# Optimization experiments

Hardware: AMD Instinct MI355X
Metric: run time of the kernel (lower is better)

Reference implementation:

```python
import jax, jax.numpy as jnp
import numpy as np

D_MODEL, NHEAD, D_HIDDEN, N_EXPERTS, TOP_K = 1024, 16, 4096, 8, 2
HEAD_DIM = D_MODEL // NHEAD
LN_EPS = 1e-5


def _layernorm(x, g, b):
    mu = jnp.mean(x, axis=-1, keepdims=True)
    var = jnp.mean((x - mu) ** 2, axis=-1, keepdims=True)
    return (x - mu) * jax.lax.rsqrt(var + LN_EPS) * g + b


def setup_inputs() -> dict:
    key = jax.random.key(0)
    ks = jax.random.split(key, 12)
    s = 0.02
    return {
        "src": jax.random.normal(ks[0], (4, 2048, D_MODEL), dtype=jnp.float32),
        "in_proj_w": jax.random.normal(ks[1], (3 * D_MODEL, D_MODEL), dtype=jnp.float32) * s,
        "in_proj_b": jnp.zeros((3 * D_MODEL,), jnp.float32),
        "out_proj_w": jax.random.normal(ks[2], (D_MODEL, D_MODEL), dtype=jnp.float32) * s,
        "out_proj_b": jnp.zeros((D_MODEL,), jnp.float32),
        "ln1_g": jnp.ones((D_MODEL,), jnp.float32),
        "ln1_b": jnp.zeros((D_MODEL,), jnp.float32),
        "gate_w": jax.random.normal(ks[3], (N_EXPERTS, D_MODEL), dtype=jnp.float32) * s,
        "gate_b": jnp.zeros((N_EXPERTS,), jnp.float32),
        "w1": jax.random.normal(ks[4], (N_EXPERTS, D_HIDDEN, D_MODEL), dtype=jnp.float32) * s,
        "b1": jnp.zeros((N_EXPERTS, D_HIDDEN), jnp.float32),
        "w2": jax.random.normal(ks[5], (N_EXPERTS, D_MODEL, D_HIDDEN), dtype=jnp.float32) * s,
        "b2": jnp.zeros((N_EXPERTS, D_MODEL), jnp.float32),
        "ln2_g": jnp.ones((D_MODEL,), jnp.float32),
        "ln2_b": jnp.zeros((D_MODEL,), jnp.float32),
    }


def _forward(src, in_proj_w, in_proj_b, out_proj_w, out_proj_b,
             ln1_g, ln1_b, gate_w, gate_b, w1, b1, w2, b2, ln2_g, ln2_b):
    B, S, D = src.shape
    # --- multihead self-attention (torch nn.MultiheadAttention semantics) ---
    qkv = src @ in_proj_w.T + in_proj_b                       # [B,S,3D]
    q, k, v = jnp.split(qkv, 3, axis=-1)
    def heads(t):
        return t.reshape(B, S, NHEAD, HEAD_DIM).transpose(0, 2, 1, 3)  # [B,H,S,hd]
    q, k, v = heads(q), heads(k), heads(v)
    scores = jnp.einsum("bhqd,bhkd->bhqk", q, k) / jnp.sqrt(jnp.float32(HEAD_DIM))
    attn = jax.nn.softmax(scores, axis=-1)
    ctx = jnp.einsum("bhqk,bhkd->bhqd", attn, v)
    ctx = ctx.transpose(0, 2, 1, 3).reshape(B, S, D)
    attn_out = ctx @ out_proj_w.T + out_proj_b
    x = _layernorm(src + attn_out, ln1_g, ln1_b)
    # --- MoE FFN: linear gate, top-k softmax routing, 2-layer ReLU experts ---
    xt = x.reshape(B * S, D)                                  # [T,D]
    gating_logits = xt @ gate_w.T + gate_b                    # [T,E]
    top_vals, top_idx = jax.lax.top_k(gating_logits, TOP_K)   # [T,k]
    top_probs = jax.nn.softmax(top_vals, axis=-1)             # [T,k]
    # dense [T,E] routing weights (zero for non-selected experts)
    weights = jnp.sum(top_probs[..., None] * jax.nn.one_hot(top_idx, N_EXPERTS, dtype=xt.dtype), axis=1)
    moe = jnp.zeros_like(xt)
    for e in range(N_EXPERTS):  # small fixed loop over experts
        h = jax.nn.relu(xt @ w1[e].T + b1[e])                 # [T,d_hidden]
        moe = moe + weights[:, e:e + 1] * (h @ w2[e].T + b2[e])
    moe = moe.reshape(B, S, D)
    out = _layernorm(x + moe, ln2_g, ln2_b)
    return out, gating_logits.reshape(B, S, N_EXPERTS)


def reference(src, in_proj_w, in_proj_b, out_proj_w, out_proj_b,
              ln1_g, ln1_b, gate_w, gate_b, w1, b1, w2, b2, ln2_g, ln2_b):
    return _forward(src, in_proj_w, in_proj_b, out_proj_w, out_proj_b,
                    ln1_g, ln1_b, gate_w, gate_b, w1, b1, w2, b2, ln2_g, ln2_b)
```

## Files before the change

kernel.cpp:

```cpp
#include <hip/hip_runtime.h>
#include <cstdint>

#define DEV static __device__ __forceinline__

typedef unsigned short u16;
typedef unsigned int   u32;
typedef __attribute__((ext_vector_type(8))) short bf16x8;
typedef __attribute__((ext_vector_type(8))) _Float16 f16x8;
typedef __attribute__((ext_vector_type(4))) float f32x4;

constexpr int TT   = 8192;
constexpr int DM   = 1024;
constexpr int DHID = 4096;
constexpr int MPAD = 17408;

constexpr size_t OFF_R0 = 0;
constexpr size_t OFF_R1 = 142606336;
constexpr size_t OFF_R2 = 178257920;
constexpr size_t OFF_R3 = 211812352;
constexpr size_t OFF_RT = 247463936;

DEV u16 f2b(float f){ u32 b = __builtin_bit_cast(u32, f); return (u16)((b + 0x7FFFu + ((b>>16)&1u))>>16); }
DEV float b2f(u16 u){ u32 b = ((u32)u)<<16; return __builtin_bit_cast(float, b); }

DEV void split2(float x, float y, u32& hi, u32& lo){
  _Float16 hx = (_Float16)x, hy = (_Float16)y;
  float rx = (x - (float)hx)*1024.f, ry = (y - (float)hy)*1024.f;
  _Float16 lx = (_Float16)rx, ly = (_Float16)ry;
  hi = (u32)__builtin_bit_cast(u16,hx) | ((u32)__builtin_bit_cast(u16,hy)<<16);
  lo = (u32)__builtin_bit_cast(u16,lx) | ((u32)__builtin_bit_cast(u16,ly)<<16);
}

DEV void stage16(const float* __restrict__ src, u16* hiB, u16* loB, int r, int c0, float scale){
  float4 v[4];
  #pragma unroll
  for (int j=0;j<4;j++) v[j] = *(const float4*)(src + c0 + 4*j);
  #pragma unroll
  for (int j=0;j<4;j++){ v[j].x*=scale; v[j].y*=scale; v[j].z*=scale; v[j].w*=scale; }
  u32 h[8], lo8[8];
  split2(v[0].x, v[0].y, h[0], lo8[0]); split2(v[0].z, v[0].w, h[1], lo8[1]);
  split2(v[1].x, v[1].y, h[2], lo8[2]); split2(v[1].z, v[1].w, h[3], lo8[3]);
  split2(v[2].x, v[2].y, h[4], lo8[4]); split2(v[2].z, v[2].w, h[5], lo8[5]);
  split2(v[3].x, v[3].y, h[6], lo8[6]); split2(v[3].z, v[3].w, h[7], lo8[7]);
  const int cb = c0>>3;
  const int i0 = r*64 + (((cb+0) ^ (r&7))<<3);
  const int i1 = r*64 + (((cb+1) ^ (r&7))<<3);
  *(uint4*)&hiB[i0] = make_uint4(h[0],h[1],h[2],h[3]);
  *(uint4*)&hiB[i1] = make_uint4(h[4],h[5],h[6],h[7]);
  *(uint4*)&loB[i0] = make_uint4(lo8[0],lo8[1],lo8[2],lo8[3]);
  *(uint4*)&loB[i1] = make_uint4(lo8[4],lo8[5],lo8[6],lo8[7]);
}

template<int RESID>
__global__ __launch_bounds__(256,2) void gemm_f16x2_kernel(
    const float* __restrict__ A, const float* __restrict__ W,
    const float* __restrict__ bias, const float* __restrict__ resid,
    float* __restrict__ C, int K, int N)
{
  __shared__ __align__(16) u16 sm[24576];
  u16* Ahi = sm;          u16* Alo = sm + 8192;
  u16* Bhi = sm + 16384;  u16* Blo = sm + 20480;
  const int m0 = blockIdx.y*128, n0 = blockIdx.x*64;
  const int t = threadIdx.x, l = t&63, w = t>>6;
  const int lr = l&15, lg = l>>4;
  const int wr = (w>>1)*64, wc = (w&1)*32;
  const int ar = t>>1, ac0 = (t&1)*32;
  const int br = t>>2, bc0 = (t&3)*16;
  f32x4 a0[4][2], a1[4][2];
  #pragma unroll
  for (int m=0;m<4;m++)
    #pragma unroll
    for (int n=0;n<2;n++){ a0[m][n]=(f32x4){0,0,0,0}; a1[m][n]=(f32x4){0,0,0,0}; }
  const float* Arow = A + (size_t)(m0+ar)*K;
  const float* Wrow = W + (size_t)(n0+br)*K;
  for (int k0=0; k0<K; k0+=64){
    __syncthreads();
    stage16(Arow + k0, Ahi, Alo, ar, ac0,      1.f);
    stage16(Arow + k0, Ahi, Alo, ar, ac0 + 16, 1.f);
    stage16(Wrow + k0, Bhi, Blo, br, bc0,      1.f);
    __syncthreads();
    #pragma unroll
    for (int s=0;s<2;s++){
      f16x8 bh[2], bl[2];
      #pragma unroll
      for (int n=0;n<2;n++){
        const int bi = (wc+16*n+lr)*64 + ((32*s + 8*lg) ^ ((lr&7)<<3));
        bh[n] = *(const f16x8*)&Bhi[bi];
        bl[n] = *(const f16x8*)&Blo[bi];
      }
      #pragma unroll
      for (int m=0;m<4;m++){
        const int ai = (wr+16*m+lr)*64 + ((32*s + 8*lg) ^ ((lr&7)<<3));
        const f16x8 ah = *(const f16x8*)&Ahi[ai];
        const f16x8 al = *(const f16x8*)&Alo[ai];
        #pragma unroll
        for (int n=0;n<2;n++){
          a0[m][n] = __builtin_amdgcn_mfma_f32_16x16x32_f16(ah, bh[n], a0[m][n], 0,0,0);
          a1[m][n] = __builtin_amdgcn_mfma_f32_16x16x32_f16(ah, bl[n], a1[m][n], 0,0,0);
          a1[m][n] = __builtin_amdgcn_mfma_f32_16x16x32_f16(al, bh[n], a1[m][n], 0,0,0);
        }
      }
    }
  }
  #pragma unroll
  for (int m=0;m<4;m++)
    #pragma unroll
    for (int n=0;n<2;n++){
      const int gn = n0 + wc + 16*n + lr;
      const float be = bias[gn];
      #pragma unroll
      for (int r=0;r<4;r++){
        const int gm = m0 + wr + 16*m + 4*lg + r;
        float v = a0[m][n][r] + a1[m][n][r]*9.765625e-4f + be;
        if (RESID) v += resid[(size_t)gm*N + gn];
        C[(size_t)gm*N + gn] = v;
      }
    }
}

__global__ __launch_bounds__(256,2) void attn_mfma_kernel(
    const float* __restrict__ qkv, float* __restrict__ ctx)
{
  __shared__ __align__(16) u16 sm[24576];
  u16* Khi = sm;          u16* Klo = sm + 4096;
  u16* Vhi = sm + 8192;   u16* Vlo = sm + 12288;
  u16* Phi = sm + 16384;  u16* Plo = sm + 20480;
  float* fsm = (float*)sm;
  const int bh = blockIdx.y, bb = bh>>4, h = bh&15;
  const int tb = bb*2048, q0 = blockIdx.x*64, go = h*64;
  const int t = threadIdx.x, l = t&63, w = t>>6;
  const int lr = l&15, lg = l>>4;
  const int sr = t>>2, sc0 = (t&3)*16;

  stage16(qkv + (size_t)(tb+q0+sr)*3072 + go, Phi, Plo, sr, sc0, 0.125f);
  __syncthreads();
  f16x8 qh[2], ql[2];
  #pragma unroll
  for (int s=0;s<2;s++){
    const int qi = (16*w+lr)*64 + ((32*s + 8*lg) ^ ((lr&7)<<3));
    qh[s] = *(const f16x8*)&Phi[qi];
    ql[s] = *(const f16x8*)&Plo[qi];
  }

  float m_ = -1e30f, l_ = 0.f;
  f32x4 c0a[4], c1a[4];
  #pragma unroll
  for (int m=0;m<4;m++){ c0a[m]=(f32x4){0,0,0,0}; c1a[m]=(f32x4){0,0,0,0}; }

  for (int kt=0; kt<32; ++kt){
    const size_t kb = (size_t)(tb + kt*64);
    __syncthreads();
    stage16(qkv + (kb+sr)*3072 + 1024 + go, Khi, Klo, sr, sc0, 1.f);
    {
      const int d = l;
      u32 vh[8], vlo[8];
      #pragma unroll
      for (int j=0;j<8;j++){
        const float f0 = qkv[(kb + w*16 + 2*j    )*3072 + 2048 + go + d];
        const float f1 = qkv[(kb + w*16 + 2*j + 1)*3072 + 2048 + go + d];
        split2(f0, f1, vh[j], vlo[j]);
      }
      const int i0 = d*64 + ((16*w + 0) ^ ((d&7)<<3));
      const int i1 = d*64 + ((16*w + 8) ^ ((d&7)<<3));
      *(uint4*)&Vhi[i0] = make_uint4(vh[0],vh[1],vh[2],vh[3]);
      *(uint4*)&Vhi[i1] = make_uint4(vh[4],vh[5],vh[6],vh[7]);
      *(uint4*)&Vlo[i0] = make_uint4(vlo[0],vlo[1],vlo[2],vlo[3]);
      *(uint4*)&Vlo[i1] = make_uint4(vlo[4],vlo[5],vlo[6],vlo[7]);
    }
    __syncthreads();
    f32x4 s0[4], s1[4];
    #pragma unroll
    for (int m=0;m<4;m++){ s0[m]=(f32x4){0,0,0,0}; s1[m]=(f32x4){0,0,0,0}; }
    #pragma unroll
    for (int s=0;s<2;s++){
      #pragma unroll
      for (int m=0;m<4;m++){
        const int ai = (16*m+lr)*64 + ((32*s + 8*lg) ^ ((lr&7)<<3));
        const f16x8 ah = *(const f16x8*)&Khi[ai];
        const f16x8 al = *(const f16x8*)&Klo[ai];
        s0[m] = __builtin_amdgcn_mfma_f32_16x16x32_f16(ah, qh[s], s0[m], 0,0,0);
        s1[m] = __builtin_amdgcn_mfma_f32_16x16x32_f16(ah, ql[s], s1[m], 0,0,0);
        s1[m] = __builtin_amdgcn_mfma_f32_16x16x32_f16(al, qh[s], s1[m], 0,0,0);
      }
    }
    float p[4][4];
    float mx = -1e30f;
    #pragma unroll
    for (int m=0;m<4;m++)
      #pragma unroll
      for (int r=0;r<4;r++){
        const float v = s0[m][r] + s1[m][r]*9.765625e-4f;
        p[m][r] = v; mx = fmaxf(mx, v);
      }
    mx = fmaxf(mx, __shfl_xor(mx,16));
    mx = fmaxf(mx, __shfl_xor(mx,32));
    const float mn = fmaxf(m_, mx);
    const float sc = __expf(m_ - mn);
    float rs = 0.f;
    #pragma unroll
    for (int m=0;m<4;m++)
      #pragma unroll
      for (int r=0;r<4;r++){ const float e = __expf(p[m][r]-mn); p[m][r]=e; rs += e; }
    rs += __shfl_xor(rs,16);
    rs += __shfl_xor(rs,32);
    l_ = l_*sc + rs; m_ = mn;
    #pragma unroll
    for (int m=0;m<4;m++){ c0a[m] *= sc; c1a[m] *= sc; }
    const int prow = 16*w + lr;
    #pragma unroll
    for (int m=0;m<4;m++){
      u32 h0,l0,h1,l1;
      split2(p[m][0], p[m][1], h0, l0);
      split2(p[m][2], p[m][3], h1, l1);
      const int pi = prow*64 + ((16*m + 4*lg) ^ ((lr&7)<<3));
      *(uint2*)&Phi[pi] = make_uint2(h0,h1);
      *(uint2*)&Plo[pi] = make_uint2(l0,l1);
    }
    #pragma unroll
    for (int s=0;s<2;s++){
      const int bi = prow*64 + ((32*s + 8*lg) ^ ((lr&7)<<3));
      const f16x8 ph = *(const f16x8*)&Phi[bi];
      const f16x8 pl = *(const f16x8*)&Plo[bi];
      #pragma unroll
      for (int m=0;m<4;m++){
        const int ai = (16*m+lr)*64 + ((32*s + 8*lg) ^ ((lr&7)<<3));
        const f16x8 vh8 = *(const f16x8*)&Vhi[ai];
        const f16x8 vl8 = *(const f16x8*)&Vlo[ai];
        c0a[m] = __builtin_amdgcn_mfma_f32_16x16x32_f16(vh8, ph, c0a[m], 0,0,0);
        c1a[m] = __builtin_amdgcn_mfma_f32_16x16x32_f16(vh8, pl, c1a[m], 0,0,0);
        c1a[m] = __builtin_amdgcn_mfma_f32_16x16x32_f16(vl8, ph, c1a[m], 0,0,0);
      }
    }
  }
  __syncthreads();
  {
    const float inv = 1.f/l_;
    const int q = 16*w + lr;
    #pragma unroll
    for (int m=0;m<4;m++)
      #pragma unroll
      for (int r=0;r<4;r++)
        fsm[q*68 + 16*m + 4*lg + r] = (c0a[m][r] + c1a[m][r]*9.765625e-4f)*inv;
  }
  __syncthreads();
  #pragma unroll
  for (int j=0;j<4;j++){
    const float4 vv = *(const float4*)&fsm[sr*68 + sc0 + 4*j];
    *(float4*)&ctx[(size_t)(tb+q0+sr)*1024 + go + sc0 + 4*j] = vv;
  }
}

__global__ __launch_bounds__(256) void ln_kernel(const float* __restrict__ in,
    const float* __restrict__ g, const float* __restrict__ b, float* __restrict__ o)
{
  const int r = blockIdx.x, t = threadIdx.x;
  const float4 v = *(const float4*)&in[(size_t)r*1024 + t*4];
  float s = v.x+v.y+v.z+v.w;
  float q = v.x*v.x + v.y*v.y + v.z*v.z + v.w*v.w;
  #pragma unroll
  for (int off=1; off<64; off<<=1){ s += __shfl_xor(s,off); q += __shfl_xor(q,off); }
  __shared__ float red[8];
  const int w = t>>6, lane = t&63;
  if (lane==0){ red[w]=s; red[4+w]=q; }
  __syncthreads();
  s = red[0]+red[1]+red[2]+red[3];
  q = red[4]+red[5]+red[6]+red[7];
  const float mu = s*(1.f/1024.f);
  const float var = q*(1.f/1024.f) - mu*mu;
  const float rstd = rsqrtf(var + 1e-5f);
  const float4 gv = *(const float4*)&g[t*4];
  const float4 bv = *(const float4*)&b[t*4];
  *(float4*)&o[(size_t)r*1024 + t*4] = make_float4(
    (v.x-mu)*rstd*gv.x + bv.x, (v.y-mu)*rstd*gv.y + bv.y,
    (v.z-mu)*rstd*gv.z + bv.z, (v.w-mu)*rstd*gv.w + bv.w);
}

__global__ __launch_bounds__(256) void gate_kernel(
    const float* __restrict__ xf, const float* __restrict__ gw, const float* __restrict__ gb,
    float* __restrict__ glog, int* __restrict__ top2e,
    float* __restrict__ p0a, float* __restrict__ p1a, int* __restrict__ counts)
{
  const int tok  = blockIdx.x*4 + (threadIdx.x>>6);
  const int lane = threadIdx.x & 63;
  float part[8] = {};
  const float* xr = xf + (size_t)tok*1024;
  #pragma unroll
  for (int kk=0; kk<16; kk++){
    const int d = kk*64 + lane;
    const float xv = xr[d];
    #pragma unroll
    for (int e=0;e<8;e++) part[e] = fmaf(xv, gw[e*1024+d], part[e]);
  }
  #pragma unroll
  for (int e=0;e<8;e++){
    float s = part[e];
    s += __shfl_xor(s,1); s += __shfl_xor(s,2); s += __shfl_xor(s,4);
    s += __shfl_xor(s,8); s += __shfl_xor(s,16); s += __shfl_xor(s,32);
    part[e] = s + gb[e];
  }
  if (lane==0){
    #pragma unroll
    for (int e=0;e<8;e++) glog[(size_t)tok*8+e] = part[e];
    float v0=-1e30f; int e0=0;
    #pragma unroll
    for (int e=0;e<8;e++) if (part[e] > v0){ v0=part[e]; e0=e; }
    float v1=-1e30f; int e1=0;
    #pragma unroll
    for (int e=0;e<8;e++) if (e!=e0 && part[e] > v1){ v1=part[e]; e1=e; }
    const float p0 = 1.f/(1.f + __expf(v1-v0));
    top2e[tok] = e0 | (e1<<4);
    p0a[tok] = p0; p1a[tok] = 1.f - p0;
    atomicAdd(&counts[e0],1); atomicAdd(&counts[e1],1);
  }
}

__global__ void route_offsets_kernel(const int* __restrict__ counts, int* __restrict__ offs,
                                     int* __restrict__ cursors, int* __restrict__ rowmap)
{
  const int t = threadIdx.x;
  if (t==0){
    int a=0;
    for (int e=0;e<8;e++){ offs[e]=a; a += (counts[e]+127)&~127; }
    offs[8]=a;
  }
  if (t<8) cursors[t]=0;
  for (int i=t;i<MPAD;i+=256) rowmap[i] = -1;
}

__global__ void route_assign_kernel(const int* __restrict__ top2e, const int* __restrict__ offs,
    int* __restrict__ cursors, int* __restrict__ rowmap, int* __restrict__ tokslot)
{
  const int tok = blockIdx.x*256 + threadIdx.x;
  const int pk = top2e[tok];
  const int e0 = pk & 15, e1 = pk >> 4;
  const int s0 = offs[e0] + atomicAdd(&cursors[e0], 1);
  const int s1 = offs[e1] + atomicAdd(&cursors[e1], 1);
  rowmap[s0] = tok; rowmap[s1] = tok;
  tokslot[2*tok] = s0; tokslot[2*tok+1] = s1;
}

__global__ __launch_bounds__(256) void gather_kernel(const int* __restrict__ rowmap,
    const float* __restrict__ xf, u16* __restrict__ xg)
{
  const int slot = blockIdx.x, t = threadIdx.x;
  u16* dst = xg + (size_t)slot*1024;
  const int r = rowmap[slot];
  if (r >= 0){
    const float4 v = *(const float4*)&xf[(size_t)r*1024 + t*4];
    uint2 p; p.x = (u32)f2b(v.x) | ((u32)f2b(v.y)<<16);
             p.y = (u32)f2b(v.z) | ((u32)f2b(v.w)<<16);
    *(uint2*)&dst[t*4] = p;
  } else {
    uint2 z; z.x=0u; z.y=0u;
    *(uint2*)&dst[t*4] = z;
  }
}

template<int KDIM, int EPI>
__global__ __launch_bounds__(256,2) void gemm_moe_kernel(
    const u16* __restrict__ A, const float* __restrict__ Wbase,
    const float* __restrict__ biasbase, u16* __restrict__ C,
    const int* __restrict__ offs, int N)
{
  constexpr int LS = 56;
  __shared__ u16 As[128*LS];
  __shared__ u16 Bs[128*LS];
  const int m0 = blockIdx.y*128, n0 = blockIdx.x*128;
  int e = 0;
  #pragma unroll
  for (int i=1;i<8;i++) if (offs[i] <= m0) e = i;
  const float* W    = Wbase + (size_t)e*N*KDIM;
  const float* bias = biasbase + (size_t)e*N;
  const int t = threadIdx.x;
  const int w = t>>6, lane = t&63;
  const int wr = (w>>1)*64, wc = (w&1)*64;
  const int lr = lane&15, lk = (lane>>4)*8;
  const int ar = t>>2, ac8 = (t&3)*8;
  const int br = t>>3, bc4 = (t&7)*4;
  f32x4 acc[4][4];
  #pragma unroll
  for (int mi=0;mi<4;mi++)
    #pragma unroll
    for (int ni=0;ni<4;ni++){ acc[mi][ni][0]=0.f; acc[mi][ni][1]=0.f; acc[mi][ni][2]=0.f; acc[mi][ni][3]=0.f; }
  for (int k0=0; k0<KDIM; k0+=32){
    __syncthreads();
    #pragma unroll
    for (int it=0; it<2; it++){
      const int r = ar + it*64;
      *(uint4*)&As[r*LS + ac8] = *(const uint4*)&A[(size_t)(m0+r)*KDIM + k0 + ac8];
    }
    #pragma unroll
    for (int it=0; it<4; it++){
      const int r = br + it*32;
      const float4 v = *(const float4*)&W[(size_t)(n0+r)*KDIM + k0 + bc4];
      uint2 p; p.x = (u32)f2b(v.x) | ((u32)f2b(v.y)<<16);
               p.y = (u32)f2b(v.z) | ((u32)f2b(v.w)<<16);
      *(uint2*)&Bs[r*LS + bc4] = p;
    }
    __syncthreads();
    bf16x8 af[4], bfr[4];
    #pragma unroll
    for (int mi=0;mi<4;mi++) af[mi]  = *(const bf16x8*)&As[(wr+mi*16+lr)*LS + lk];
    #pragma unroll
    for (int ni=0;ni<4;ni++) bfr[ni] = *(const bf16x8*)&Bs[(wc+ni*16+lr)*LS + lk];
    #pragma unroll
    for (int mi=0;mi<4;mi++)
      #pragma unroll
      for (int ni=0;ni<4;ni++)
        acc[mi][ni] = __builtin_amdgcn_mfma_f32_16x16x32_bf16(af[mi], bfr[ni], acc[mi][ni], 0,0,0);
  }
  const int lr4 = (lane>>4)*4, lc = lane&15;
  #pragma unroll
  for (int mi=0;mi<4;mi++)
    #pragma unroll
    for (int ni=0;ni<4;ni++){
      const int gn = n0 + wc + ni*16 + lc;
      const float be = bias[gn];
      #pragma unroll
      for (int j=0;j<4;j++){
        const int gm = m0 + wr + mi*16 + lr4 + j;
        float v = acc[mi][ni][j] + be;
        if (EPI==0) v = fmaxf(v, 0.f);
        C[(size_t)gm*N + gn] = f2b(v);
      }
    }
}

__global__ __launch_bounds__(256) void combine_ln2_kernel(
    const float* __restrict__ xf, const u16* __restrict__ y, const int* __restrict__ tokslot,
    const float* __restrict__ p0a, const float* __restrict__ p1a,
    const float* __restrict__ g, const float* __restrict__ b, float* __restrict__ o)
{
  const int tok = blockIdx.x, t = threadIdx.x;
  const int s0 = tokslot[2*tok], s1 = tokslot[2*tok+1];
  const float w0 = p0a[tok], w1 = p1a[tok];
  const float4 xv = *(const float4*)&xf[(size_t)tok*1024 + t*4];
  const uint2 ya = *(const uint2*)&y[(size_t)s0*1024 + t*4];
  const uint2 yb = *(const uint2*)&y[(size_t)s1*1024 + t*4];
  const float va[4] = {b2f((u16)(ya.x&0xFFFF)), b2f((u16)(ya.x>>16)),
                       b2f((u16)(ya.y&0xFFFF)), b2f((u16)(ya.y>>16))};
  const float vb[4] = {b2f((u16)(yb.x&0xFFFF)), b2f((u16)(yb.x>>16)),
                       b2f((u16)(yb.y&0xFFFF)), b2f((u16)(yb.y>>16))};
  const float xe[4] = {xv.x, xv.y, xv.z, xv.w};
  float vv[4];
  #pragma unroll
  for (int i=0;i<4;i++) vv[i] = xe[i] + w0*va[i] + w1*vb[i];
  float s = vv[0]+vv[1]+vv[2]+vv[3];
  float q = vv[0]*vv[0]+vv[1]*vv[1]+vv[2]*vv[2]+vv[3]*vv[3];
  #pragma unroll
  for (int off=1; off<64; off<<=1){ s += __shfl_xor(s,off); q += __shfl_xor(q,off); }
  __shared__ float red[8];
  const int w = t>>6, lane = t&63;
  if (lane==0){ red[w]=s; red[4+w]=q; }
  __syncthreads();
  s = red[0]+red[1]+red[2]+red[3];
  q = red[4]+red[5]+red[6]+red[7];
  const float mu = s*(1.f/1024.f);
  const float var = q*(1.f/1024.f) - mu*mu;
  const float rstd = rsqrtf(var + 1e-5f);
  const float4 gv = *(const float4*)&g[t*4];
  const float4 bv = *(const float4*)&b[t*4];
  *(float4*)&o[(size_t)tok*1024 + t*4] = make_float4(
    (vv[0]-mu)*rstd*gv.x + bv.x, (vv[1]-mu)*rstd*gv.y + bv.y,
    (vv[2]-mu)*rstd*gv.z + bv.z, (vv[3]-mu)*rstd*gv.w + bv.w);
}

extern "C" void kernel_launch(void* const* d_in, const int* in_sizes, int n_in,
                              void* d_out, int out_size, void* d_ws, size_t ws_size,
                              hipStream_t stream)
{
  const float* src  = (const float*)d_in[0];
  const float* inw  = (const float*)d_in[1];
  const float* inb  = (const float*)d_in[2];
  const float* ow   = (const float*)d_in[3];
  const float* ob   = (const float*)d_in[4];
  const float* ln1g = (const float*)d_in[5];
  const float* ln1b = (const float*)d_in[6];
  const float* gw   = (const float*)d_in[7];
  const float* gb   = (const float*)d_in[8];
  const float* w1   = (const float*)d_in[9];
  const float* b1   = (const float*)d_in[10];
  const float* w2   = (const float*)d_in[11];
  const float* b2   = (const float*)d_in[12];
  const float* ln2g = (const float*)d_in[13];
  const float* ln2b = (const float*)d_in[14];

  float* out  = (float*)d_out;
  float* glog = out + (size_t)TT*DM;

  char* ws = (char*)d_ws;
  float* qkvf    = (float*)(ws + OFF_R0);
  float* attnout = (float*)(ws + OFF_R0);
  u16*   hbuf    = (u16*)  (ws + OFF_R0);
  float* ctxf    = (float*)(ws + OFF_R1);
  u16*   ybuf    = (u16*)  (ws + OFF_R1);
  float* xf      = (float*)(ws + OFF_R2);
  u16*   xg      = (u16*)  (ws + OFF_R3);
  int*   top2e   = (int*)  (ws + OFF_RT);
  float* p0a     = (float*)(ws + OFF_RT + 32768);
  float* p1a     = (float*)(ws + OFF_RT + 65536);
  int*   counts  = (int*)  (ws + OFF_RT + 98304);
  int*   offs    = (int*)  (ws + OFF_RT + 98336);
  int*   cursors = (int*)  (ws + OFF_RT + 98400);
  int*   rowmap  = (int*)  (ws + OFF_RT + 98432);
  int*   tokslot = (int*)  (ws + OFF_RT + 168064);

  hipMemsetAsync(counts, 0, 8*sizeof(int), stream);

  gemm_f16x2_kernel<0><<<dim3(48,64),256,0,stream>>>(src, inw, inb, nullptr, qkvf, 1024, 3072);
  attn_mfma_kernel<<<dim3(32,64),256,0,stream>>>(qkvf, ctxf);
  gemm_f16x2_kernel<1><<<dim3(16,64),256,0,stream>>>(ctxf, ow, ob, src, attnout, 1024, 1024);
  ln_kernel<<<8192,256,0,stream>>>(attnout, ln1g, ln1b, xf);
  gate_kernel<<<2048,256,0,stream>>>(xf, gw, gb, glog, top2e, p0a, p1a, counts);
  route_offsets_kernel<<<1,256,0,stream>>>(counts, offs, cursors, rowmap);
  route_assign_kernel<<<32,256,0,stream>>>(top2e, offs, cursors, rowmap, tokslot);
  gather_kernel<<<MPAD,256,0,stream>>>(rowmap, xf, xg);
  gemm_moe_kernel<1024,0><<<dim3(32,136),256,0,stream>>>(xg, w1, b1, hbuf, offs, DHID);
  gemm_moe_kernel<4096,1><<<dim3(8,136),256,0,stream>>>(hbuf, w2, b2, ybuf, offs, DM);
  combine_ln2_kernel<<<8192,256,0,stream>>>(xf, ybuf, tokslot, p0a, p1a, ln2g, ln2b, out);
}
```

Baseline: 1.821 ms.

## Pre-split fp16 hi/lo operands once and stage via global_load_lds in attention GEMMs

Adds prep kernels that split src, in_proj and out_proj weights into pre-swizzled fp16 hi/lo arrays, and has the QKV GEMM epilogue emit split, swizzled Q/K plus an fp32 V that a transpose kernel turns into split V^T. The GEMMs and attention kernel then stage tiles straight from global to LDS with global_load_lds, with no per-tile conversion in the inner loop. The attention kernel writes its context already split for the out-projection. The cost is extra launches and extra workspace traffic for the split copies, including re-splitting the constant weights on every call.

Result: faster. 1.671 ms (-8.3%).

```diff
diff --git a/kernel.cpp b/kernel.cpp
--- a/kernel.cpp
+++ b/kernel.cpp
@@ -14,11 +14,27 @@
 constexpr int DHID = 4096;
 constexpr int MPAD = 17408;
 
-constexpr size_t OFF_R0 = 0;
-constexpr size_t OFF_R1 = 142606336;
-constexpr size_t OFF_R2 = 178257920;
-constexpr size_t OFF_R3 = 211812352;
-constexpr size_t OFF_RT = 247463936;
+constexpr size_t O_HBUF = 0;
+constexpr size_t O_XG   = 142606336;
+constexpr size_t O_YBUF = 178257920;
+constexpr size_t O_XF   = 213909504;
+constexpr size_t O_RT   = 247463936;
+constexpr size_t O_SRCH = 0;
+constexpr size_t O_SRCL = 16777216;
+constexpr size_t O_INWH = 33554432;
+constexpr size_t O_INWL = 39845888;
+constexpr size_t O_OWH  = 46137344;
+constexpr size_t O_OWL  = 48234496;
+constexpr size_t O_QH   = 50331648;
+constexpr size_t O_QL   = 67108864;
+constexpr size_t O_KH   = 83886080;
+constexpr size_t O_KL   = 100663296;
+constexpr size_t O_VF   = 117440512;
+constexpr size_t O_VTH  = 150994944;
+constexpr size_t O_VTL  = 167772160;
+constexpr size_t O_CTXH = 184549376;
+constexpr size_t O_CTXL = 201326592;
+constexpr size_t O_AOUT = 0;
 
 DEV u16 f2b(float f){ u32 b = __builtin_bit_cast(u32, f); return (u16)((b + 0x7FFFu + ((b>>16)&1u))>>16); }
 DEV float b2f(u16 u){ u32 b = ((u32)u)<<16; return __builtin_bit_cast(float, b); }
@@ -30,69 +46,127 @@
   hi = (u32)__builtin_bit_cast(u16,hx) | ((u32)__builtin_bit_cast(u16,hy)<<16);
   lo = (u32)__builtin_bit_cast(u16,lx) | ((u32)__builtin_bit_cast(u16,ly)<<16);
 }
-
-DEV void stage16(const float* __restrict__ src, u16* hiB, u16* loB, int r, int c0, float scale){
-  float4 v[4];
-  #pragma unroll
-  for (int j=0;j<4;j++) v[j] = *(const float4*)(src + c0 + 4*j);
-  #pragma unroll
-  for (int j=0;j<4;j++){ v[j].x*=scale; v[j].y*=scale; v[j].z*=scale; v[j].w*=scale; }
-  u32 h[8], lo8[8];
-  split2(v[0].x, v[0].y, h[0], lo8[0]); split2(v[0].z, v[0].w, h[1], lo8[1]);
-  split2(v[1].x, v[1].y, h[2], lo8[2]); split2(v[1].z, v[1].w, h[3], lo8[3]);
-  split2(v[2].x, v[2].y, h[4], lo8[4]); split2(v[2].z, v[2].w, h[5], lo8[5]);
-  split2(v[3].x, v[3].y, h[6], lo8[6]); split2(v[3].z, v[3].w, h[7], lo8[7]);
-  const int cb = c0>>3;
-  const int i0 = r*64 + (((cb+0) ^ (r&7))<<3);
-  const int i1 = r*64 + (((cb+1) ^ (r&7))<<3);
-  *(uint4*)&hiB[i0] = make_uint4(h[0],h[1],h[2],h[3]);
-  *(uint4*)&hiB[i1] = make_uint4(h[4],h[5],h[6],h[7]);
-  *(uint4*)&loB[i0] = make_uint4(lo8[0],lo8[1],lo8[2],lo8[3]);
-  *(uint4*)&loB[i1] = make_uint4(lo8[4],lo8[5],lo8[6],lo8[7]);
-}
-
-template<int RESID>
-__global__ __launch_bounds__(256,2) void gemm_f16x2_kernel(
-    const float* __restrict__ A, const float* __restrict__ W,
+DEV void split1(float x, u16& h, u16& l){
+  _Float16 hx = (_Float16)x;
+  float rx = (x - (float)hx)*1024.f;
+  h = __builtin_bit_cast(u16, hx);
+  l = __builtin_bit_cast(u16, (_Float16)rx);
+}
+
+DEV void gld16(const u16* g, u16* l){
+  __builtin_amdgcn_global_load_lds(
+    (const __attribute__((address_space(1))) void*)g,
+    (__attribute__((address_space(3))) void*)l, 16, 0, 0);
+}
+
+__global__ __launch_bounds__(256) void prep_split_kernel(
+    const float* __restrict__ src, u16* __restrict__ hi, u16* __restrict__ lo)
+{
+  const int g = blockIdx.x*256 + threadIdx.x;
+  const int r = g >> 7;
+  const int ci = g & 127;
+  const float4 v0 = *(const float4*)&src[(size_t)r*1024 + ci*8];
+  const float4 v1 = *(const float4*)&src[(size_t)r*1024 + ci*8 + 4];
+  u32 h[4], l4[4];
+  split2(v0.x,v0.y,h[0],l4[0]); split2(v0.z,v0.w,h[1],l4[1]);
+  split2(v1.x,v1.y,h[2],l4[2]); split2(v1.z,v1.w,h[3],l4[3]);
+  const int co = (ci & ~7) | ((ci ^ r) & 7);
+  *(uint4*)&hi[(size_t)r*1024 + co*8] = make_uint4(h[0],h[1],h[2],h[3]);
+  *(uint4*)&lo[(size_t)r*1024 + co*8] = make_uint4(l4[0],l4[1],l4[2],l4[3]);
+}
+
+__global__ __launch_bounds__(256) void prep_vt_kernel(
+    const float* __restrict__ Vf, u16* __restrict__ VTh, u16* __restrict__ VTl)
+{
+  __shared__ float fsm[64*65];
+  const int bh = blockIdx.x, st = blockIdx.y;
+  const int bb = bh>>4, h = bh&15, go = h*64;
+  const int s0 = bb*2048 + st*64;
+  const int t = threadIdx.x;
+  {
+    const int r = t>>2, c0 = (t&3)*16;
+    #pragma unroll
+    for (int j=0;j<4;j++){
+      const float4 v = *(const float4*)&Vf[(size_t)(s0+r)*1024 + go + c0 + 4*j];
+      fsm[r*65 + c0 + 4*j+0]=v.x; fsm[r*65 + c0 + 4*j+1]=v.y;
+      fsm[r*65 + c0 + 4*j+2]=v.z; fsm[r*65 + c0 + 4*j+3]=v.w;
+    }
+  }
+  __syncthreads();
+  const int d = t>>2, qs = t&3;
+  #pragma unroll
+  for (int j2=0;j2<2;j2++){
+    const int q = qs*2 + j2;
+    float v[8];
+    #pragma unroll
+    for (int jj=0;jj<8;jj++) v[jj] = fsm[(q*8+jj)*65 + d];
+    u32 h0,h1,h2,h3,l0,l1,l2,l3;
+    split2(v[0],v[1],h0,l0); split2(v[2],v[3],h1,l1);
+    split2(v[4],v[5],h2,l2); split2(v[6],v[7],h3,l3);
+    const int cst = q ^ (d&7);
+    const size_t base = (size_t)(bh*64 + d)*2048 + st*64 + cst*8;
+    *(uint4*)&VTh[base] = make_uint4(h0,h1,h2,h3);
+    *(uint4*)&VTl[base] = make_uint4(l0,l1,l2,l3);
+  }
+}
+
+template<int EPI>
+__global__ __launch_bounds__(256,2) void gemm_pair_kernel(
+    const u16* __restrict__ Ahi, const u16* __restrict__ Alo,
+    const u16* __restrict__ Bhi, const u16* __restrict__ Blo,
     const float* __restrict__ bias, const float* __restrict__ resid,
-    float* __restrict__ C, int K, int N)
+    float* __restrict__ outf,
+    u16* __restrict__ Qh, u16* __restrict__ Ql,
+    u16* __restrict__ Kh, u16* __restrict__ Kl, float* __restrict__ Vf,
+    int K, int N)
 {
   __shared__ __align__(16) u16 sm[24576];
-  u16* Ahi = sm;          u16* Alo = sm + 8192;
-  u16* Bhi = sm + 16384;  u16* Blo = sm + 20480;
+  u16* As_hi = sm;
+  u16* As_lo = sm + 8192;
+  u16* Bs_hi = sm + 16384;
+  u16* Bs_lo = sm + 20480;
   const int m0 = blockIdx.y*128, n0 = blockIdx.x*64;
   const int t = threadIdx.x, l = t&63, w = t>>6;
   const int lr = l&15, lg = l>>4;
   const int wr = (w>>1)*64, wc = (w&1)*32;
-  const int ar = t>>1, ac0 = (t&1)*32;
-  const int br = t>>2, bc0 = (t&3)*16;
+  const int srow = w*8 + (l>>3);
+  const int sch  = l&7;
   f32x4 a0[4][2], a1[4][2];
   #pragma unroll
   for (int m=0;m<4;m++)
     #pragma unroll
     for (int n=0;n<2;n++){ a0[m][n]=(f32x4){0,0,0,0}; a1[m][n]=(f32x4){0,0,0,0}; }
-  const float* Arow = A + (size_t)(m0+ar)*K;
-  const float* Wrow = W + (size_t)(n0+br)*K;
   for (int k0=0; k0<K; k0+=64){
     __syncthreads();
-    stage16(Arow + k0, Ahi, Alo, ar, ac0,      1.f);
-    stage16(Arow + k0, Ahi, Alo, ar, ac0 + 16, 1.f);
-    stage16(Wrow + k0, Bhi, Blo, br, bc0,      1.f);
+    #pragma unroll
+    for (int op=0; op<4; ++op){
+      const int r = op*32 + srow;
+      const size_t src = (size_t)(m0+r)*K + k0 + sch*8;
+      gld16(&Ahi[src], &As_hi[(op*32 + w*8)*64]);
+      gld16(&Alo[src], &As_lo[(op*32 + w*8)*64]);
+    }
+    #pragma unroll
+    for (int op=0; op<2; ++op){
+      const int r = op*32 + srow;
+      const size_t src = (size_t)(n0+r)*K + k0 + sch*8;
+      gld16(&Bhi[src], &Bs_hi[(op*32 + w*8)*64]);
+      gld16(&Blo[src], &Bs_lo[(op*32 + w*8)*64]);
+    }
     __syncthreads();
     #pragma unroll
     for (int s=0;s<2;s++){
       f16x8 bh[2], bl[2];
       #pragma unroll
       for (int n=0;n<2;n++){
-        const int bi = (wc+16*n+lr)*64 + ((32*s + 8*lg) ^ ((lr&7)<<3));
-        bh[n] = *(const f16x8*)&Bhi[bi];
-        bl[n] = *(const f16x8*)&Blo[bi];
+        const int bi = (wc+16*n+lr)*64 + (((4*s+lg) ^ (lr&7))<<3);
+        bh[n] = *(const f16x8*)&Bs_hi[bi];
+        bl[n] = *(const f16x8*)&Bs_lo[bi];
       }
       #pragma unroll
       for (int m=0;m<4;m++){
-        const int ai = (wr+16*m+lr)*64 + ((32*s + 8*lg) ^ ((lr&7)<<3));
-        const f16x8 ah = *(const f16x8*)&Ahi[ai];
-        const f16x8 al = *(const f16x8*)&Alo[ai];
+        const int ai = (wr+16*m+lr)*64 + (((4*s+lg) ^ (lr&7))<<3);
+        const f16x8 ah = *(const f16x8*)&As_hi[ai];
+        const f16x8 al = *(const f16x8*)&As_lo[ai];
         #pragma unroll
         for (int n=0;n<2;n++){
           a0[m][n] = __builtin_amdgcn_mfma_f32_16x16x32_f16(ah, bh[n], a0[m][n], 0,0,0);
@@ -103,43 +177,64 @@
     }
   }
   #pragma unroll
-  for (int m=0;m<4;m++)
-    #pragma unroll
-    for (int n=0;n<2;n++){
-      const int gn = n0 + wc + 16*n + lr;
-      const float be = bias[gn];
+  for (int n2=0;n2<2;n2++){
+    const int gn = n0 + wc + 16*n2 + lr;
+    const float be = bias[gn];
+    #pragma unroll
+    for (int m=0;m<4;m++){
       #pragma unroll
       for (int r=0;r<4;r++){
         const int gm = m0 + wr + 16*m + 4*lg + r;
-        float v = a0[m][n][r] + a1[m][n][r]*9.765625e-4f + be;
-        if (RESID) v += resid[(size_t)gm*N + gn];
-        C[(size_t)gm*N + gn] = v;
+        float v = a0[m][n2][r] + a1[m][n2][r]*9.765625e-4f + be;
+        if (EPI==0){
+          if (gn < 1024){
+            u16 hh,ll; split1(v*0.125f, hh, ll);
+            Qh[(size_t)gm*1024 + gn] = hh; Ql[(size_t)gm*1024 + gn] = ll;
+          } else if (gn < 2048){
+            const int c = gn - 1024;
+            const int cst = (c & ~63) | ((((c>>3) ^ gm) & 7)<<3) | (c & 7);
+            u16 hh,ll; split1(v, hh, ll);
+            Kh[(size_t)gm*1024 + cst] = hh; Kl[(size_t)gm*1024 + cst] = ll;
+          } else {
+            Vf[(size_t)gm*1024 + (gn-2048)] = v;
+          }
+        } else {
+          outf[(size_t)gm*N + gn] = v + resid[(size_t)gm*N + gn];
+        }
       }
     }
+  }
 }
 
 __global__ __launch_bounds__(256,2) void attn_mfma_kernel(
-    const float* __restrict__ qkv, float* __restrict__ ctx)
+    const u16* __restrict__ Qhp, const u16* __restrict__ Qlp,
+    const u16* __restrict__ Khp, const u16* __restrict__ Klp,
+    const u16* __restrict__ VTh, const u16* __restrict__ VTl,
+    u16* __restrict__ ctxh, u16* __restrict__ ctxl)
 {
   __shared__ __align__(16) u16 sm[24576];
-  u16* Khi = sm;          u16* Klo = sm + 4096;
-  u16* Vhi = sm + 8192;   u16* Vlo = sm + 12288;
-  u16* Phi = sm + 16384;  u16* Plo = sm + 20480;
+  u16* Khs = sm;
+  u16* Kls = sm + 4096;
+  u16* Vhs = sm + 8192;
+  u16* Vls = sm + 12288;
+  u16* Phs = sm + 16384;
+  u16* Pls = sm + 20480;
   float* fsm = (float*)sm;
   const int bh = blockIdx.y, bb = bh>>4, h = bh&15;
   const int tb = bb*2048, q0 = blockIdx.x*64, go = h*64;
   const int t = threadIdx.x, l = t&63, w = t>>6;
   const int lr = l&15, lg = l>>4;
-  const int sr = t>>2, sc0 = (t&3)*16;
-
-  stage16(qkv + (size_t)(tb+q0+sr)*3072 + go, Phi, Plo, sr, sc0, 0.125f);
-  __syncthreads();
+  const int srow = w*8 + (l>>3);
+  const int sch  = l&7;
+
   f16x8 qh[2], ql[2];
-  #pragma unroll
-  for (int s=0;s<2;s++){
-    const int qi = (16*w+lr)*64 + ((32*s + 8*lg) ^ ((lr&7)<<3));
-    qh[s] = *(const f16x8*)&Phi[qi];
-    ql[s] = *(const f16x8*)&Plo[qi];
+  {
+    const size_t qr = (size_t)(tb + q0 + 16*w + lr)*1024 + go;
+    #pragma unroll
+    for (int s=0;s<2;s++){
+      qh[s] = *(const f16x8*)&Qhp[qr + 32*s + 8*lg];
+      ql[s] = *(const f16x8*)&Qlp[qr + 32*s + 8*lg];
+    }
   }
 
   float m_ = -1e30f, l_ = 0.f;
@@ -148,24 +243,17 @@
   for (int m=0;m<4;m++){ c0a[m]=(f32x4){0,0,0,0}; c1a[m]=(f32x4){0,0,0,0}; }
 
   for (int kt=0; kt<32; ++kt){
-    const size_t kb = (size_t)(tb + kt*64);
+    const int kb = tb + kt*64;
     __syncthreads();
-    stage16(qkv + (kb+sr)*3072 + 1024 + go, Khi, Klo, sr, sc0, 1.f);
-    {
-      const int d = l;
-      u32 vh[8], vlo[8];
-      #pragma unroll
-      for (int j=0;j<8;j++){
-        const float f0 = qkv[(kb + w*16 + 2*j    )*3072 + 2048 + go + d];
-        const float f1 = qkv[(kb + w*16 + 2*j + 1)*3072 + 2048 + go + d];
-        split2(f0, f1, vh[j], vlo[j]);
-      }
-      const int i0 = d*64 + ((16*w + 0) ^ ((d&7)<<3));
-      const int i1 = d*64 + ((16*w + 8) ^ ((d&7)<<3));
-      *(uint4*)&Vhi[i0] = make_uint4(vh[0],vh[1],vh[2],vh[3]);
-      *(uint4*)&Vhi[i1] = make_uint4(vh[4],vh[5],vh[6],vh[7]);
-      *(uint4*)&Vlo[i0] = make_uint4(vlo[0],vlo[1],vlo[2],vlo[3]);
-      *(uint4*)&Vlo[i1] = make_uint4(vlo[4],vlo[5],vlo[6],vlo[7]);
+    #pragma unroll
+    for (int op=0; op<2; ++op){
+      const int r = op*32 + srow;
+      const size_t ksrc = (size_t)(kb + r)*1024 + go + sch*8;
+      const size_t vsrc = (size_t)(bh*64 + r)*2048 + kt*64 + sch*8;
+      gld16(&Khp[ksrc], &Khs[(op*32 + w*8)*64]);
+      gld16(&Klp[ksrc], &Kls[(op*32 + w*8)*64]);
+      gld16(&VTh[vsrc], &Vhs[(op*32 + w*8)*64]);
+      gld16(&VTl[vsrc], &Vls[(op*32 + w*8)*64]);
     }
     __syncthreads();
     f32x4 s0[4], s1[4];
@@ -175,9 +263,9 @@
     for (int s=0;s<2;s++){
       #pragma unroll
       for (int m=0;m<4;m++){
-        const int ai = (16*m+lr)*64 + ((32*s + 8*lg) ^ ((lr&7)<<3));
-        const f16x8 ah = *(const f16x8*)&Khi[ai];
-        const f16x8 al = *(const f16x8*)&Klo[ai];
+        const int ai = (16*m+lr)*64 + (((4*s+lg) ^ (lr&7))<<3);
+        const f16x8 ah = *(const f16x8*)&Khs[ai];
+        const f16x8 al = *(const f16x8*)&Kls[ai];
         s0[m] = __builtin_amdgcn_mfma_f32_16x16x32_f16(ah, qh[s], s0[m], 0,0,0);
         s1[m] = __builtin_amdgcn_mfma_f32_16x16x32_f16(ah, ql[s], s1[m], 0,0,0);
         s1[m] = __builtin_amdgcn_mfma_f32_16x16x32_f16(al, qh[s], s1[m], 0,0,0);
@@ -213,19 +301,19 @@
       split2(p[m][0], p[m][1], h0, l0);
       split2(p[m][2], p[m][3], h1, l1);
       const int pi = prow*64 + ((16*m + 4*lg) ^ ((lr&7)<<3));
-      *(uint2*)&Phi[pi] = make_uint2(h0,h1);
-      *(uint2*)&Plo[pi] = make_uint2(l0,l1);
+      *(uint2*)&Phs[pi] = make_uint2(h0,h1);
+      *(uint2*)&Pls[pi] = make_uint2(l0,l1);
     }
     #pragma unroll
     for (int s=0;s<2;s++){
       const int bi = prow*64 + ((32*s + 8*lg) ^ ((lr&7)<<3));
-      const f16x8 ph = *(const f16x8*)&Phi[bi];
-      const f16x8 pl = *(const f16x8*)&Plo[bi];
+      const f16x8 ph = *(const f16x8*)&Phs[bi];
+      const f16x8 pl = *(const f16x8*)&Pls[bi];
       #pragma unroll
       for (int m=0;m<4;m++){
-        const int ai = (16*m+lr)*64 + ((32*s + 8*lg) ^ ((lr&7)<<3));
-        const f16x8 vh8 = *(const f16x8*)&Vhi[ai];
-        const f16x8 vl8 = *(const f16x8*)&Vlo[ai];
+        const int ai = (16*m+lr)*64 + (((4*s+lg) ^ (lr&7))<<3);
+        const f16x8 vh8 = *(const f16x8*)&Vhs[ai];
+        const f16x8 vl8 = *(const f16x8*)&Vls[ai];
         c0a[m] = __builtin_amdgcn_mfma_f32_16x16x32_f16(vh8, ph, c0a[m], 0,0,0);
         c1a[m] = __builtin_amdgcn_mfma_f32_16x16x32_f16(vh8, pl, c1a[m], 0,0,0);
         c1a[m] = __builtin_amdgcn_mfma_f32_16x16x32_f16(vl8, ph, c1a[m], 0,0,0);
@@ -243,10 +331,23 @@
         fsm[q*68 + 16*m + 4*lg + r] = (c0a[m][r] + c1a[m][r]*9.765625e-4f)*inv;
   }
   __syncthreads();
-  #pragma unroll
-  for (int j=0;j<4;j++){
-    const float4 vv = *(const float4*)&fsm[sr*68 + sc0 + 4*j];
-    *(float4*)&ctx[(size_t)(tb+q0+sr)*1024 + go + sc0 + 4*j] = vv;
+  {
+    const int sr2 = t>>2, qs2 = t&3;
+    const int row = tb + q0 + sr2;
+    #pragma unroll
+    for (int j2=0;j2<2;j2++){
+      const int cch = qs2*2 + j2;
+      float v[8];
+      #pragma unroll
+      for (int jj=0;jj<8;jj++) v[jj] = fsm[sr2*68 + cch*8 + jj];
+      u32 h0,h1,h2,h3,l0,l1,l2,l3;
+      split2(v[0],v[1],h0,l0); split2(v[2],v[3],h1,l1);
+      split2(v[4],v[5],h2,l2); split2(v[6],v[7],h3,l3);
+      const int cst = cch ^ (row&7);
+      const size_t base = (size_t)row*1024 + go + cst*8;
+      *(uint4*)&ctxh[base] = make_uint4(h0,h1,h2,h3);
+      *(uint4*)&ctxl[base] = make_uint4(l0,l1,l2,l3);
+    }
   }
 }
 
@@ -489,27 +590,46 @@
   float* glog = out + (size_t)TT*DM;
 
   char* ws = (char*)d_ws;
-  float* qkvf    = (float*)(ws + OFF_R0);
-  float* attnout = (float*)(ws + OFF_R0);
-  u16*   hbuf    = (u16*)  (ws + OFF_R0);
-  float* ctxf    = (float*)(ws + OFF_R1);
-  u16*   ybuf    = (u16*)  (ws + OFF_R1);
-  float* xf      = (float*)(ws + OFF_R2);
-  u16*   xg      = (u16*)  (ws + OFF_R3);
-  int*   top2e   = (int*)  (ws + OFF_RT);
-  float* p0a     = (float*)(ws + OFF_RT + 32768);
-  float* p1a     = (float*)(ws + OFF_RT + 65536);
-  int*   counts  = (int*)  (ws + OFF_RT + 98304);
-  int*   offs    = (int*)  (ws + OFF_RT + 98336);
-  int*   cursors = (int*)  (ws + OFF_RT + 98400);
-  int*   rowmap  = (int*)  (ws + OFF_RT + 98432);
-  int*   tokslot = (int*)  (ws + OFF_RT + 168064);
+  u16*   hbuf    = (u16*)  (ws + O_HBUF);
+  u16*   xg      = (u16*)  (ws + O_XG);
+  u16*   ybuf    = (u16*)  (ws + O_YBUF);
+  float* xf      = (float*)(ws + O_XF);
+  u16*   srch    = (u16*)  (ws + O_SRCH);
+  u16*   srcl    = (u16*)  (ws + O_SRCL);
+  u16*   inwh    = (u16*)  (ws + O_INWH);
+  u16*   inwl    = (u16*)  (ws + O_INWL);
+  u16*   owh     = (u16*)  (ws + O_OWH);
+  u16*   owl     = (u16*)  (ws + O_OWL);
+  u16*   Qh      = (u16*)  (ws + O_QH);
+  u16*   Ql      = (u16*)  (ws + O_QL);
+  u16*   Kh      = (u16*)  (ws + O_KH);
+  u16*   Kl      = (u16*)  (ws + O_KL);
+  float* Vf      = (float*)(ws + O_VF);
+  u16*   VTh     = (u16*)  (ws + O_VTH);
+  u16*   VTl     = (u16*)  (ws + O_VTL);
+  u16*   ctxh    = (u16*)  (ws + O_CTXH);
+  u16*   ctxl    = (u16*)  (ws + O_CTXL);
+  float* attnout = (float*)(ws + O_AOUT);
+  int*   top2e   = (int*)  (ws + O_RT);
+  float* p0a     = (float*)(ws + O_RT + 32768);
+  float* p1a     = (float*)(ws + O_RT + 65536);
+  int*   counts  = (int*)  (ws + O_RT + 98304);
+  int*   offs    = (int*)  (ws + O_RT + 98336);
+  int*   cursors = (int*)  (ws + O_RT + 98400);
+  int*   rowmap  = (int*)  (ws + O_RT + 98432);
+  int*   tokslot = (int*)  (ws + O_RT + 168064);
 
   hipMemsetAsync(counts, 0, 8*sizeof(int), stream);
 
-  gemm_f16x2_kernel<0><<<dim3(48,64),256,0,stream>>>(src, inw, inb, nullptr, qkvf, 1024, 3072);
-  attn_mfma_kernel<<<dim3(32,64),256,0,stream>>>(qkvf, ctxf);
-  gemm_f16x2_kernel<1><<<dim3(16,64),256,0,stream>>>(ctxf, ow, ob, src, attnout, 1024, 1024);
+  prep_split_kernel<<<4096,256,0,stream>>>(src, srch, srcl);
+  prep_split_kernel<<<1536,256,0,stream>>>(inw, inwh, inwl);
+  prep_split_kernel<<< 512,256,0,stream>>>(ow,  owh,  owl);
+  gemm_pair_kernel<0><<<dim3(48,64),256,0,stream>>>(srch, srcl, inwh, inwl, inb,
+      nullptr, nullptr, Qh, Ql, Kh, Kl, Vf, 1024, 3072);
+  prep_vt_kernel<<<dim3(64,32),256,0,stream>>>(Vf, VTh, VTl);
+  attn_mfma_kernel<<<dim3(32,64),256,0,stream>>>(Qh, Ql, Kh, Kl, VTh, VTl, ctxh, ctxl);
+  gemm_pair_kernel<1><<<dim3(16,64),256,0,stream>>>(ctxh, ctxl, owh, owl, ob,
+      src, attnout, nullptr, nullptr, nullptr, nullptr, nullptr, 1024, 1024);
   ln_kernel<<<8192,256,0,stream>>>(attnout, ln1g, ln1b, xf);
   gate_kernel<<<2048,256,0,stream>>>(xf, gw, gb, glog, top2e, p0a, p1a, counts);
   route_offsets_kernel<<<1,256,0,stream>>>(counts, offs, cursors, rowmap);
```
